# Optimization experiments

Hardware: AMD Instinct MI355X
Metric: run time of the kernel (lower is better)

The kernel has to match this reference:

```python
import jax, jax.numpy as jnp
import numpy as np

DIM = 256
DIM_HEAD = 32
HEADS = DIM // DIM_HEAD
WINDOW = 7
REGS = 1
N = WINDOW + REGS  # 8
B = 32768
NUM_REL = 2 * WINDOW - 1  # 13; table has NUM_REL+1 = 14 rows


def _rel_pos_indices():
    pos = np.arange(WINDOW)
    rel = pos[:, None] - pos[None, :] + (WINDOW - 1)  # [7,7] in [0,12]
    out = np.full((N, N), NUM_REL, dtype=np.int64)    # pad registers with index 13
    out[REGS:, REGS:] = rel
    return jnp.asarray(out)


def setup_inputs() -> dict:
    key = jax.random.key(0)
    ks = jax.random.split(key, 4)
    x = jax.random.normal(ks[0], (B, N, DIM), dtype=jnp.float32)
    ln_w = jnp.ones((DIM,), jnp.float32)
    ln_b = jnp.zeros((DIM,), jnp.float32)
    w_qkv = jax.random.normal(ks[1], (DIM, 3 * DIM), jnp.float32) * 0.02
    w_out = jax.random.normal(ks[2], (DIM, DIM), jnp.float32) * 0.02
    rel_bias_table = jax.random.normal(ks[3], (NUM_REL + 1, HEADS), jnp.float32) * 0.02
    return {"x": x, "ln_w": ln_w, "ln_b": ln_b, "w_qkv": w_qkv,
            "w_out": w_out, "rel_bias_table": rel_bias_table,
            "rel_pos_indices": _rel_pos_indices()}


def reference(x, ln_w, ln_b, w_qkv, w_out, rel_bias_table, rel_pos_indices):
    b, n, dim = x.shape
    h, d = HEADS, DIM_HEAD
    scale = d ** -0.5
    # LayerNorm (eps=1e-5, as torch default)
    mu = jnp.mean(x, axis=-1, keepdims=True)
    var = jnp.mean((x - mu) ** 2, axis=-1, keepdims=True)
    xn = (x - mu) * jax.lax.rsqrt(var + 1e-5) * ln_w + ln_b
    qkv = xn @ w_qkv                                   # [b, n, 3*dim]
    q, k, v = jnp.split(qkv, 3, axis=-1)
    split_heads = lambda t: t.reshape(b, n, h, d).transpose(0, 2, 1, 3)  # b h n d
    q, k, v = map(split_heads, (q, k, v))
    sim = jnp.einsum('bhid,bhjd->bhij', q * scale, k)  # [b, h, n, n]
    bias = rel_bias_table[rel_pos_indices]             # [n, n, h]
    sim = sim + bias.transpose(2, 0, 1)[None]          # broadcast over batch
    attn = jax.nn.softmax(sim, axis=-1)
    out = jnp.einsum('bhij,bhjd->bhid', attn, v)       # [b, h, n, d]
    out = out.transpose(0, 2, 1, 3).reshape(b, n, dim)
    return out @ w_out
```

## Files before the change

### kernel.cpp

```cpp
#include <hip/hip_runtime.h>

#define NH 8
#define DH 32
#define ROWS 128
#define SLD 36
#define VTLD 20

typedef __attribute__((ext_vector_type(8))) short bf16x8;
typedef __attribute__((ext_vector_type(4))) short bf16x4;
typedef __attribute__((ext_vector_type(4))) float f32x4;

__device__ __forceinline__ unsigned short f2bf(float f) {
  unsigned u = __float_as_uint(f);
  u = (u + 0x7fffu + ((u >> 16) & 1u)) >> 16;
  return (unsigned short)u;
}

__device__ __forceinline__ void gload16(const void* g, void* l) {
  __builtin_amdgcn_global_load_lds((const __attribute__((address_space(1))) void*)g,
                                   (__attribute__((address_space(3))) void*)l, 16, 0, 0);
}

__global__ void prep_kernel(const float* __restrict__ wqkv, const float* __restrict__ wout,
                            const float* __restrict__ table, const int* __restrict__ relidx,
                            unsigned short* __restrict__ wqkvF, unsigned short* __restrict__ woutF,
                            float* __restrict__ biasM) {
  __shared__ float T[64][65];
  const int b = blockIdx.x, tid = threadIdx.x;
  if (b == 64) {
    for (int e = tid; e < 512; e += 256) {
      const int hh = e >> 6, ij = e & 63;
      biasM[e] = table[relidx[ij] * NH + hh];
    }
    return;
  }
  const float* src; int N, k0, n0; bool isqkv;
  if (b < 48) { src = wqkv; N = 768; k0 = (b / 12) * 64; n0 = (b % 12) * 64; isqkv = true; }
  else { const int bb = b - 48; src = wout; N = 256; k0 = (bb >> 2) * 64; n0 = (bb & 3) * 64; isqkv = false; }
  const int c = tid & 63, rb = (tid >> 6) * 16;
  #pragma unroll
  for (int p = 0; p < 16; ++p)
    T[c][rb + p] = src[(size_t)(k0 + rb + p) * N + n0 + c];
  __syncthreads();
  #pragma unroll
  for (int it = 0; it < 2; ++it) {
    const int chunk = tid * 2 + it;
    const int n_loc = chunk >> 3, kc = chunk & 7;
    const int n = n0 + n_loc, k = k0 + kc * 8;
    if (isqkv) {
      const int l15 = n & 15, quad = (k >> 3) & 3, kk = k >> 5;
      const float sc = (n < 256) ? 0.17677669529663687f : 1.f;
      union { unsigned short e[8]; uint4 q; } u;
      #pragma unroll
      for (int e = 0; e < 8; ++e) u.e[e] = f2bf(T[n_loc][kc * 8 + e] * sc);
      const int sec = n >> 8, hh = (n >> 5) & 7, tu = (n >> 4) & 1;
      const size_t faddr = (size_t)((((hh * 6 + sec * 2 + tu) * 8 + kk) * 64 + quad * 16 + l15) * 8);
      *(uint4*)&wqkvF[faddr] = u.q;
    } else {
      const int ntg = n >> 4, nl = n & 15;
      #pragma unroll
      for (int g = 0; g < 2; ++g) {
        const int k4 = k + g * 4;
        const int cc = k4 >> 4, qd = (k4 >> 2) & 3;
        const int flat = (ntg >> 2) * 64 + cc * 4 + (ntg & 3);
        ushort4 u4;
        u4.x = f2bf(T[n_loc][kc * 8 + g * 4 + 0]);
        u4.y = f2bf(T[n_loc][kc * 8 + g * 4 + 1]);
        u4.z = f2bf(T[n_loc][kc * 8 + g * 4 + 2]);
        u4.w = f2bf(T[n_loc][kc * 8 + g * 4 + 3]);
        *(ushort4*)&woutF[(size_t)((flat * 64 + qd * 16 + nl) * 4)] = u4;
      }
    }
  }
}

__global__ __launch_bounds__(256, 2)
void attn_main(const float* __restrict__ x,
               const float* __restrict__ ln_w,
               const float* __restrict__ ln_b,
               const unsigned short* __restrict__ wqkvF,
               const unsigned short* __restrict__ woutF,
               const float* __restrict__ biasM,
               float* __restrict__ out) {
  __shared__ unsigned short s_stage[96 * 256];
  __shared__ unsigned short s_q[ROWS * SLD];
  __shared__ unsigned short s_k[ROWS * SLD];
  __shared__ unsigned short s_vT[8 * 32 * VTLD];
  __shared__ float s_bias[NH * 64];

  const int tid  = threadIdx.x;
  const int w    = tid >> 6;
  const int lane = tid & 63;
  const int l15  = lane & 15;
  const int quad = lane >> 4;
  const int row0 = blockIdx.x * ROWS;

  auto stage_qkv = [&](int hh) {
    #pragma unroll
    for (int it = 0; it < 12; ++it)
      gload16(wqkvF + (size_t)(hh * 48 + w * 12 + it) * 512 + lane * 8,
              &s_stage[(w * 12 + it) * 512]);
  };
  auto stage_out = [&](int pp) {
    #pragma unroll
    for (int it = 0; it < 8; ++it)
      gload16(woutF + (size_t)pp * 16384 + (w * 8 + it) * 512 + lane * 8,
              &s_stage[(w * 8 + it) * 512]);
  };

  stage_qkv(0);
  for (int e = tid; e < 512; e += 256) s_bias[e] = biasM[e];

  bf16x8 afrag[2][8];
  #pragma unroll
  for (int mt = 0; mt < 2; ++mt) {
    const int lrow = (2 * w + mt) * 16 + l15;
    const float* xr = x + (size_t)(row0 + lrow) * 256;
    float4 xv[16];
    float sum = 0.f, ss = 0.f;
    #pragma unroll
    for (int kk = 0; kk < 8; ++kk) {
      #pragma unroll
      for (int i = 0; i < 2; ++i) {
        const float4 v = *(const float4*)(xr + kk * 32 + quad * 8 + i * 4);
        xv[kk * 2 + i] = v;
        sum += v.x + v.y + v.z + v.w;
        ss  += v.x * v.x + v.y * v.y + v.z * v.z + v.w * v.w;
      }
    }
    sum += __shfl_xor(sum, 16); ss += __shfl_xor(ss, 16);
    sum += __shfl_xor(sum, 32); ss += __shfl_xor(ss, 32);
    const float mean = sum * (1.f / 256.f);
    const float var  = ss * (1.f / 256.f) - mean * mean;
    const float rstd = rsqrtf(var + 1e-5f);
    #pragma unroll
    for (int kk = 0; kk < 8; ++kk) {
      union { bf16x8 v; unsigned short e[8]; } pk;
      #pragma unroll
      for (int i = 0; i < 2; ++i) {
        const float4 g   = *(const float4*)(ln_w + kk * 32 + quad * 8 + i * 4);
        const float4 bta = *(const float4*)(ln_b + kk * 32 + quad * 8 + i * 4);
        const float4 v = xv[kk * 2 + i];
        pk.e[i * 4 + 0] = f2bf((v.x - mean) * rstd * g.x + bta.x);
        pk.e[i * 4 + 1] = f2bf((v.y - mean) * rstd * g.y + bta.y);
        pk.e[i * 4 + 2] = f2bf((v.z - mean) * rstd * g.z + bta.z);
        pk.e[i * 4 + 3] = f2bf((v.w - mean) * rstd * g.w + bta.w);
      }
      afrag[mt][kk] = pk.v;
    }
  }
  __syncthreads();

  bf16x4 ao[2][16];
  const f32x4 fz = {0.f, 0.f, 0.f, 0.f};

  #pragma unroll
  for (int h = 0; h < NH; ++h) {
    f32x4 acc[2][6];
    #pragma unroll
    for (int mt = 0; mt < 2; ++mt)
      #pragma unroll
      for (int t = 0; t < 6; ++t) acc[mt][t] = fz;
    #pragma unroll
    for (int kk = 0; kk < 8; ++kk) {
      const bf16x8 a0 = afrag[0][kk];
      const bf16x8 a1 = afrag[1][kk];
      #pragma unroll
      for (int t = 0; t < 6; ++t) {
        const bf16x8 bfr = *(const bf16x8*)&s_stage[(t * 8 + kk) * 512 + lane * 8];
        acc[0][t] = __builtin_amdgcn_mfma_f32_16x16x32_bf16(a0, bfr, acc[0][t], 0, 0, 0);
        acc[1][t] = __builtin_amdgcn_mfma_f32_16x16x32_bf16(a1, bfr, acc[1][t], 0, 0, 0);
      }
    }
    __syncthreads();
    if (h < NH - 1) stage_qkv(h + 1); else stage_out(0);

    #pragma unroll
    for (int mt = 0; mt < 2; ++mt) {
      const int rowb = (2 * w + mt) * 16 + quad * 4;
      #pragma unroll
      for (int u = 0; u < 2; ++u) {
        #pragma unroll
        for (int r = 0; r < 4; ++r) {
          s_q[(rowb + r) * SLD + u * 16 + l15] = f2bf(acc[mt][u][r]);
          s_k[(rowb + r) * SLD + u * 16 + l15] = f2bf(acc[mt][2 + u][r]);
        }
        ushort4 v4;
        v4.x = f2bf(acc[mt][4 + u][0]); v4.y = f2bf(acc[mt][4 + u][1]);
        v4.z = f2bf(acc[mt][4 + u][2]); v4.w = f2bf(acc[mt][4 + u][3]);
        *(ushort4*)&s_vT[((2 * w + mt) * 32 + u * 16 + l15) * VTLD + quad * 4] = v4;
      }
    }

    {
      const float4 bb = *(const float4*)&s_bias[h * 64 + (l15 & 7) * 8 + (quad & 1) * 4];
      const bool valid = (quad >> 1) == (l15 >> 3);
      #pragma unroll
      for (int mt = 0; mt < 2; ++mt) {
        const int tb = (2 * w + mt) * 16;
        const bf16x8 kf = *(const bf16x8*)&s_k[(tb + l15) * SLD + quad * 8];
        const bf16x8 qf = *(const bf16x8*)&s_q[(tb + l15) * SLD + quad * 8];
        const f32x4 st = __builtin_amdgcn_mfma_f32_16x16x32_bf16(kf, qf, fz, 0, 0, 0);
        const float e0 = __expf(fminf(valid ? st[0] + bb.x : -3.0e38f, 60.f));
        const float e1 = __expf(fminf(valid ? st[1] + bb.y : -3.0e38f, 60.f));
        const float e2 = __expf(fminf(valid ? st[2] + bb.z : -3.0e38f, 60.f));
        const float e3 = __expf(fminf(valid ? st[3] + bb.w : -3.0e38f, 60.f));
        float s4 = e0 + e1 + e2 + e3;
        s4 += __shfl_xor(s4, 16);
        s4 += __shfl_xor(s4, 32);
        const float inv = 1.f / fmaxf(s4, 1e-30f);
        union { bf16x4 v; unsigned short e[4]; } pf;
        pf.e[0] = f2bf(e0); pf.e[1] = f2bf(e1); pf.e[2] = f2bf(e2); pf.e[3] = f2bf(e3);
        #pragma unroll
        for (int u = 0; u < 2; ++u) {
          const bf16x4 vf = *(const bf16x4*)&s_vT[((2 * w + mt) * 32 + u * 16 + l15) * VTLD + quad * 4];
          const f32x4 ot = __builtin_amdgcn_mfma_f32_16x16x16bf16_1k(vf, pf.v, fz, 0, 0, 0);
          union { bf16x4 v; unsigned short e[4]; } po;
          po.e[0] = f2bf(ot[0] * inv); po.e[1] = f2bf(ot[1] * inv);
          po.e[2] = f2bf(ot[2] * inv); po.e[3] = f2bf(ot[3] * inv);
          ao[mt][2 * h + u] = po.v;
        }
      }
    }
    __syncthreads();
  }

  for (int p = 0; p < 4; ++p) {
    f32x4 oacc[2][4];
    #pragma unroll
    for (int mt = 0; mt < 2; ++mt)
      #pragma unroll
      for (int nt = 0; nt < 4; ++nt) oacc[mt][nt] = fz;

    #pragma unroll
    for (int c = 0; c < 16; ++c) {
      const bf16x4 a0 = ao[0][c];
      const bf16x4 a1 = ao[1][c];
      #pragma unroll
      for (int nt = 0; nt < 4; ++nt) {
        const bf16x4 bfr = *(const bf16x4*)&s_stage[(c * 4 + nt) * 256 + lane * 4];
        oacc[0][nt] = __builtin_amdgcn_mfma_f32_16x16x16bf16_1k(a0, bfr, oacc[0][nt], 0, 0, 0);
        oacc[1][nt] = __builtin_amdgcn_mfma_f32_16x16x16bf16_1k(a1, bfr, oacc[1][nt], 0, 0, 0);
      }
    }
    if (p < 3) {
      __syncthreads();
      stage_out(p + 1);
    }
    #pragma unroll
    for (int mt = 0; mt < 2; ++mt)
      #pragma unroll
      for (int nt = 0; nt < 4; ++nt)
        #pragma unroll
        for (int r = 0; r < 4; ++r) {
          const int grow = row0 + (2 * w + mt) * 16 + quad * 4 + r;
          out[(size_t)grow * 256 + p * 64 + nt * 16 + l15] = oacc[mt][nt][r];
        }
    if (p < 3) __syncthreads();
  }
}

extern "C" void kernel_launch(void* const* d_in, const int* in_sizes, int n_in,
                              void* d_out, int out_size, void* d_ws, size_t ws_size,
                              hipStream_t stream) {
  const float* x      = (const float*)d_in[0];
  const float* ln_w   = (const float*)d_in[1];
  const float* ln_b   = (const float*)d_in[2];
  const float* wqkv   = (const float*)d_in[3];
  const float* wout   = (const float*)d_in[4];
  const float* table  = (const float*)d_in[5];
  const int*   relidx = (const int*)d_in[6];
  float* out = (float*)d_out;

  unsigned short* wqkvF = (unsigned short*)d_ws;
  unsigned short* woutF = wqkvF + 768 * 256;
  float* biasM = (float*)(woutF + 256 * 256);

  prep_kernel<<<65, 256, 0, stream>>>(wqkv, wout, table, relidx, wqkvF, woutF, biasM);
  attn_main<<<2048, 256, 0, stream>>>(x, ln_w, ln_b, wqkvF, woutF, biasM, out);
}
```

Baseline: 606.1 us.

## Double-buffer weight staging and use 512-thread blocks covering 256 rows

Doubles the block to 512 threads handling 256 rows, so each head's QKV weight slice staged in shared memory is reused by twice as many rows. It also splits the staging buffer into two ping-pong buffers so the next head's (or next output panel's) weights are prefetched while the current MFMAs run, removing one barrier per iteration. In exchange, occupancy drops to one block per CU with a larger LDS footprint. Correctness depends on the existing end-of-loop barriers ordering each prefetch against reads of the other buffer.

```diff
diff --git a/kernel.cpp b/kernel.cpp
--- a/kernel.cpp
+++ b/kernel.cpp
@@ -2,7 +2,7 @@
 
 #define NH 8
 #define DH 32
-#define ROWS 128
+#define ROWS 256
 #define SLD 36
 #define VTLD 20
 
@@ -74,7 +74,7 @@
   }
 }
 
-__global__ __launch_bounds__(256, 2)
+__global__ __launch_bounds__(512, 1)
 void attn_main(const float* __restrict__ x,
                const float* __restrict__ ln_w,
                const float* __restrict__ ln_b,
@@ -82,10 +82,11 @@
                const unsigned short* __restrict__ woutF,
                const float* __restrict__ biasM,
                float* __restrict__ out) {
-  __shared__ unsigned short s_stage[96 * 256];
+  __shared__ unsigned short s_stage0[48 * 512];
+  __shared__ unsigned short s_stage1[48 * 512];
   __shared__ unsigned short s_q[ROWS * SLD];
   __shared__ unsigned short s_k[ROWS * SLD];
-  __shared__ unsigned short s_vT[8 * 32 * VTLD];
+  __shared__ unsigned short s_vT[16 * 32 * VTLD];
   __shared__ float s_bias[NH * 64];
 
   const int tid  = threadIdx.x;
@@ -95,21 +96,21 @@
   const int quad = lane >> 4;
   const int row0 = blockIdx.x * ROWS;
 
-  auto stage_qkv = [&](int hh) {
-    #pragma unroll
-    for (int it = 0; it < 12; ++it)
-      gload16(wqkvF + (size_t)(hh * 48 + w * 12 + it) * 512 + lane * 8,
-              &s_stage[(w * 12 + it) * 512]);
+  auto stage_qkv = [&](int hh, unsigned short* buf) {
+    #pragma unroll
+    for (int it = 0; it < 6; ++it)
+      gload16(wqkvF + (size_t)(hh * 48 + w * 6 + it) * 512 + lane * 8,
+              &buf[(w * 6 + it) * 512]);
   };
-  auto stage_out = [&](int pp) {
-    #pragma unroll
-    for (int it = 0; it < 8; ++it)
-      gload16(woutF + (size_t)pp * 16384 + (w * 8 + it) * 512 + lane * 8,
-              &s_stage[(w * 8 + it) * 512]);
+  auto stage_out = [&](int pp, unsigned short* buf) {
+    #pragma unroll
+    for (int it = 0; it < 4; ++it)
+      gload16(woutF + (size_t)pp * 16384 + (w * 4 + it) * 512 + lane * 8,
+              &buf[(w * 4 + it) * 512]);
   };
 
-  stage_qkv(0);
-  for (int e = tid; e < 512; e += 256) s_bias[e] = biasM[e];
+  stage_qkv(0, s_stage0);
+  s_bias[tid] = biasM[tid];
 
   bf16x8 afrag[2][8];
   #pragma unroll
@@ -156,6 +157,10 @@
 
   #pragma unroll
   for (int h = 0; h < NH; ++h) {
+    unsigned short* bufC = (h & 1) ? s_stage1 : s_stage0;
+    unsigned short* bufN = (h & 1) ? s_stage0 : s_stage1;
+    if (h < NH - 1) stage_qkv(h + 1, bufN); else stage_out(0, bufN);
+
     f32x4 acc[2][6];
     #pragma unroll
     for (int mt = 0; mt < 2; ++mt)
@@ -167,13 +172,11 @@
       const bf16x8 a1 = afrag[1][kk];
       #pragma unroll
       for (int t = 0; t < 6; ++t) {
-        const bf16x8 bfr = *(const bf16x8*)&s_stage[(t * 8 + kk) * 512 + lane * 8];
+        const bf16x8 bfr = *(const bf16x8*)&bufC[(t * 8 + kk) * 512 + lane * 8];
         acc[0][t] = __builtin_amdgcn_mfma_f32_16x16x32_bf16(a0, bfr, acc[0][t], 0, 0, 0);
         acc[1][t] = __builtin_amdgcn_mfma_f32_16x16x32_bf16(a1, bfr, acc[1][t], 0, 0, 0);
       }
     }
-    __syncthreads();
-    if (h < NH - 1) stage_qkv(h + 1); else stage_out(0);
 
     #pragma unroll
     for (int mt = 0; mt < 2; ++mt) {
@@ -225,7 +228,12 @@
     __syncthreads();
   }
 
+  #pragma unroll
   for (int p = 0; p < 4; ++p) {
+    unsigned short* bufC = (p & 1) ? s_stage1 : s_stage0;
+    unsigned short* bufN = (p & 1) ? s_stage0 : s_stage1;
+    if (p < 3) stage_out(p + 1, bufN);
+
     f32x4 oacc[2][4];
     #pragma unroll
     for (int mt = 0; mt < 2; ++mt)
@@ -238,14 +246,10 @@
       const bf16x4 a1 = ao[1][c];
       #pragma unroll
       for (int nt = 0; nt < 4; ++nt) {
-        const bf16x4 bfr = *(const bf16x4*)&s_stage[(c * 4 + nt) * 256 + lane * 4];
+        const bf16x4 bfr = *(const bf16x4*)&bufC[(c * 4 + nt) * 256 + lane * 4];
         oacc[0][nt] = __builtin_amdgcn_mfma_f32_16x16x16bf16_1k(a0, bfr, oacc[0][nt], 0, 0, 0);
         oacc[1][nt] = __builtin_amdgcn_mfma_f32_16x16x16bf16_1k(a1, bfr, oacc[1][nt], 0, 0, 0);
       }
-    }
-    if (p < 3) {
-      __syncthreads();
-      stage_out(p + 1);
     }
     #pragma unroll
     for (int mt = 0; mt < 2; ++mt)
@@ -277,5 +281,5 @@
   float* biasM = (float*)(woutF + 256 * 256);
 
   prep_kernel<<<65, 256, 0, stream>>>(wqkv, wout, table, relidx, wqkvF, woutF, biasM);
-  attn_main<<<2048, 256, 0, stream>>>(x, ln_w, ln_b, wqkvF, woutF, biasM, out);
-}
+  attn_main<<<1024, 512, 0, stream>>>(x, ln_w, ln_b, wqkvF, woutF, biasM, out);
+}
```

Measured after the change: 673.1 us. 1.11x slower.
